# Performance work log

Hardware: AMD Instinct MI355X
Metric: run time of the kernel (lower is better)

## Reference

```python
import jax, jax.numpy as jnp
import numpy as np


def _l2norm(t, axis=-1, eps=1e-12):
    # matches torch F.normalize: x / max(||x||, eps)
    n = jnp.sqrt(jnp.sum(t * t, axis=axis, keepdims=True))
    return t / jnp.maximum(n, eps)


def setup_inputs() -> dict:
    key = jax.random.key(0)
    ks = jax.random.split(key, 5)
    B, N, C, H = 16, 4096, 768, 12
    x = jax.random.normal(ks[0], (B, N, C), dtype=jnp.float32)
    Wqkv = jax.random.normal(ks[1], (C, 3 * C), dtype=jnp.float32) * (C ** -0.5)
    bqkv = jax.random.normal(ks[2], (3 * C,), dtype=jnp.float32) * 0.02
    Wproj = jax.random.normal(ks[3], (C, C), dtype=jnp.float32) * (C ** -0.5)
    bproj = jax.random.normal(ks[4], (C,), dtype=jnp.float32) * 0.02
    temperature = jnp.ones((H, 1, 1), dtype=jnp.float32)
    return {"x": x, "Wqkv": Wqkv, "bqkv": bqkv, "Wproj": Wproj,
            "bproj": bproj, "temperature": temperature}


def reference(x, Wqkv, bqkv, Wproj, bproj, temperature):
    B, N, C = x.shape
    H = temperature.shape[0]
    Dh = C // H
    qkv = x @ Wqkv + bqkv                      # [B,N,3C]
    qkv = qkv.reshape(B, N, 3, H, Dh)
    # -> [3,B,H,Dh,N] (channels-as-tokens layout)
    qkv = jnp.transpose(qkv, (2, 0, 3, 4, 1))
    q, k, v = qkv[0], qkv[1], qkv[2]           # each [B,H,Dh,N]
    q = _l2norm(q, axis=-1)
    k = _l2norm(k, axis=-1)
    # cross-covariance over channels: [B,H,Dh,Dh]
    attn = jnp.einsum('bhdn,bhen->bhde', q, k) * temperature
    attn = jax.nn.softmax(attn, axis=-1)
    out = jnp.einsum('bhde,bhen->bhdn', attn, v)  # [B,H,Dh,N]
    out = jnp.transpose(out, (0, 3, 1, 2)).reshape(B, N, C)
    return out @ Wproj + bproj
```

## Files before the change

kernel.cpp:

```cpp
#include <hip/hip_runtime.h>

typedef __bf16 bf16x8 __attribute__((ext_vector_type(8)));
typedef float  f32x4  __attribute__((ext_vector_type(4)));
typedef unsigned short u16x8 __attribute__((ext_vector_type(8)));
typedef unsigned short u16x4 __attribute__((ext_vector_type(4)));

#define MFMA16(a, b, c) __builtin_amdgcn_mfma_f32_16x16x32_bf16((a), (b), (c), 0, 0, 0)

#define GLOAD16(g, l) __builtin_amdgcn_global_load_lds( \
    (const __attribute__((address_space(1))) void*)(g),  \
    (__attribute__((address_space(3))) void*)(l), 16, 0, 0)

__device__ __forceinline__ float bf2f(unsigned short u) {
    unsigned int x = ((unsigned int)u) << 16;
    return __builtin_bit_cast(float, x);
}
__device__ __forceinline__ unsigned short f2bf(float f) {
    unsigned int x = __builtin_bit_cast(unsigned int, f);
    x = x + 0x7FFFu + ((x >> 16) & 1u);
    return (unsigned short)(x >> 16);
}
__device__ __forceinline__ bool is_f32(const unsigned short* tf) { return tf[0] == 0; }
__device__ __forceinline__ float ldscal(const void* p, int i, bool f32m) {
    return f32m ? ((const float*)p)[i] : bf2f(((const unsigned short*)p)[i]);
}

__global__ __launch_bounds__(256)
void tr_dual(const void* __restrict__ in_, unsigned short* __restrict__ xb,
             unsigned short* __restrict__ xbT, const unsigned short* __restrict__ tf)
{
    __shared__ unsigned short T[64 * 72];
    const bool f32m = is_f32(tf);
    const int tx = blockIdx.x % 12;
    const int ty = blockIdx.x / 12;
    const int r0 = ty * 64, c0 = tx * 64;
    const int t = threadIdx.x;
#pragma unroll
    for (int s = 0; s < 2; ++s) {
        const int idx = t + s * 256;
        const int rr = idx >> 3;
        const int cc = (idx & 7) * 8;
        u16x8 v;
        if (f32m) {
            const float* inf = (const float*)in_;
            f32x4 a = *(const f32x4*)&inf[(size_t)(r0 + rr) * 768 + c0 + cc];
            f32x4 b = *(const f32x4*)&inf[(size_t)(r0 + rr) * 768 + c0 + cc + 4];
#pragma unroll
            for (int j = 0; j < 4; ++j) { v[j] = f2bf(a[j]); v[4 + j] = f2bf(b[j]); }
        } else {
            v = *(const u16x8*)&((const unsigned short*)in_)[(size_t)(r0 + rr) * 768 + c0 + cc];
        }
        *(u16x8*)&xb[(size_t)(r0 + rr) * 768 + c0 + cc] = v;
#pragma unroll
        for (int j = 0; j < 8; ++j) T[(cc + j) * 72 + rr] = v[j];
    }
    __syncthreads();
#pragma unroll
    for (int s = 0; s < 2; ++s) {
        const int idx = t + s * 256;
        const int cc = idx >> 3;
        const int rr = (idx & 7) * 8;
        u16x8 v = *(const u16x8*)&T[cc * 72 + rr];
        *(u16x8*)&xbT[(size_t)(c0 + cc) * 65536 + r0 + rr] = v;
    }
}

__global__ __launch_bounds__(256)
void tr_conv(const void* __restrict__ in_, unsigned short* __restrict__ out,
             int R, int C, int istride, const unsigned short* __restrict__ tf)
{
    __shared__ unsigned short T[64 * 72];
    const bool f32m = is_f32(tf);
    const int nct = C >> 6;
    const int tx = blockIdx.x % nct;
    const int ty = blockIdx.x / nct;
    const int r0 = ty * 64, c0 = tx * 64;
    const int t = threadIdx.x;
#pragma unroll
    for (int s = 0; s < 2; ++s) {
        const int idx = t + s * 256;
        const int rr = idx >> 3;
        const int cc = (idx & 7) * 8;
        unsigned short v[8];
        if (f32m) {
            const float* inf = (const float*)in_;
            f32x4 a = *(const f32x4*)&inf[(size_t)(r0 + rr) * istride + c0 + cc];
            f32x4 b = *(const f32x4*)&inf[(size_t)(r0 + rr) * istride + c0 + cc + 4];
#pragma unroll
            for (int j = 0; j < 4; ++j) { v[j] = f2bf(a[j]); v[4 + j] = f2bf(b[j]); }
        } else {
            u16x8 a = *(const u16x8*)&((const unsigned short*)in_)[(size_t)(r0 + rr) * istride + c0 + cc];
#pragma unroll
            for (int j = 0; j < 8; ++j) v[j] = a[j];
        }
#pragma unroll
        for (int j = 0; j < 8; ++j) T[(cc + j) * 72 + rr] = v[j];
    }
    __syncthreads();
#pragma unroll
    for (int s = 0; s < 2; ++s) {
        const int idx = t + s * 256;
        const int cc = idx >> 3;
        const int rr = (idx & 7) * 8;
        u16x8 v = *(const u16x8*)&T[cc * 72 + rr];
        *(u16x8*)&out[(size_t)(c0 + cc) * R + r0 + rr] = v;
    }
}

__global__ __launch_bounds__(256)
void conv_wv(const void* __restrict__ Wqkv, unsigned short* __restrict__ Wv_bf,
             const unsigned short* __restrict__ tf)
{
    const bool f32m = is_f32(tf);
    const int t = blockIdx.x * 256 + threadIdx.x;
    const int c = t / 96;
    const int e0 = (t % 96) * 8;
    u16x8 v;
    if (f32m) {
        const float* p = (const float*)Wqkv + (size_t)c * 2304 + 1536 + e0;
        f32x4 a = *(const f32x4*)p;
        f32x4 b = *(const f32x4*)(p + 4);
#pragma unroll
        for (int j = 0; j < 4; ++j) { v[j] = f2bf(a[j]); v[4 + j] = f2bf(b[j]); }
    } else {
        v = *(const u16x8*)&((const unsigned short*)Wqkv)[(size_t)c * 2304 + 1536 + e0];
    }
    *(u16x8*)&Wv_bf[(size_t)c * 768 + e0] = v;
}

__global__ __launch_bounds__(256)
void colsum(const unsigned short* __restrict__ xbT, float* __restrict__ s)
{
    const int b = blockIdx.x / 12;
    const int jg = blockIdx.x % 12;
    const int tid = threadIdx.x;
    const int d = tid >> 2;
    const int seg = tid & 3;
    const int j = jg * 64 + d;
    const unsigned short* p = xbT + (size_t)j * 65536 + b * 4096 + seg * 1024;
    float acc = 0.f;
    for (int i = 0; i < 128; ++i) {
        u16x8 v = *(const u16x8*)&p[i * 8];
#pragma unroll
        for (int k = 0; k < 8; ++k) acc += bf2f(v[k]);
    }
    acc += __shfl_xor(acc, 1);
    acc += __shfl_xor(acc, 2);
    if (seg == 0) s[b * 768 + j] = acc;
}

template<int MODE>
__global__ __launch_bounds__(512, 2)
void gemm256(const unsigned short* __restrict__ A,
             const unsigned short* __restrict__ BT,
             const float* __restrict__ bias,
             unsigned short* __restrict__ o0,
             float* __restrict__ oF,
             const unsigned short* __restrict__ tf)
{
    constexpr int NT = (MODE == 3) ? 64 : 12;
    constexpr size_t LDA = (MODE == 3) ? 65536 : 768;
    constexpr size_t LDB = (MODE == 3) ? 65536 : 768;
    __shared__ __align__(16) char SM[131072];

    const bool f32m = is_f32(tf);
    const int tid  = threadIdx.x;
    const int wave = tid >> 6;
    const int lane = tid & 63;
    const int wm   = wave >> 2;
    const int wn   = wave & 3;
    const int lr   = lane & 15;
    const int lq   = lane >> 4;
    const int lrh  = lr >> 1;
    const int pA   = (((lr & 1) << 2) | lq) ^ lrh;

    const int per = gridDim.x >> 3;
    const int wg  = (blockIdx.x & 7) * per + (blockIdx.x >> 3);
    int b = 0, mt, nt;
    if (MODE == 3)      { b = wg / 9;  const int r = wg % 9;  mt = r / 3; nt = r % 3; }
    else if (MODE == 4) { b = wg / 18; const int r = wg % 18; mt = r / 3; nt = r % 3; }
    else                { mt = wg / 3; nt = wg % 3; }
    const size_t m0 = (size_t)mt * 256;
    const int n0 = nt * 256;

    const unsigned short* Ab;
    const unsigned short* Bb;
    if (MODE == 3)      { Ab = A + m0 * LDA + (size_t)b * 4096;
                          Bb = A + (size_t)n0 * LDA + (size_t)b * 4096; }
    else if (MODE == 4) { Ab = A + m0 * LDA;
                          Bb = BT + (size_t)b * 589824 + (size_t)n0 * LDB; }
    else if (MODE == 1) { Ab = A + m0 * LDA;
                          Bb = BT + (m0 >> 12) * (size_t)589824 + (size_t)n0 * LDB; }
    else                { Ab = A + m0 * LDA;
                          Bb = BT + (size_t)n0 * LDB; }

    f32x4 zero = {0.f, 0.f, 0.f, 0.f};
    f32x4 acc[8][4];
#pragma unroll
    for (int i = 0; i < 8; ++i)
#pragma unroll
        for (int j = 0; j < 4; ++j) acc[i][j] = zero;

    auto STAGE_EV = [&](int mat, int kh, int t) {
        const unsigned short* g = mat ? Bb : Ab;
        const size_t ld = mat ? LDB : LDA;
        char* dst = SM + (t & 1) * 65536 + mat * 32768 + kh * 16384;
#pragma unroll
        for (int ev = 0; ev < 2; ++ev) {
            const int c = ev * 512 + tid;
            const int rp = c >> 3;
            const int chunk = (c & 7) ^ (rp & 7);
            const int srow = rp * 2 + (chunk >> 2);
            const int sk = kh * 32 + (chunk & 3) * 8;
            GLOAD16(g + (size_t)srow * ld + t * 64 + sk, dst + c * 16);
        }
    };

    STAGE_EV(0, 0, 0); STAGE_EV(1, 0, 0);
    STAGE_EV(0, 1, 0); STAGE_EV(1, 1, 0);
    STAGE_EV(0, 0, 1); STAGE_EV(1, 0, 1);

    bf16x8 af[4], bfr[4];

#define READ_B(ks) do { \
    _Pragma("unroll") for (int ni = 0; ni < 4; ++ni) \
        bfr[ni] = *(const bf16x8*)(lb + (ks) * 16384 + (wn * 32 + ni * 8 + lrh) * 128 + pA * 16); } while (0)
#define READ_A(mh, ks) do { \
    _Pragma("unroll") for (int mi = 0; mi < 4; ++mi) \
        af[mi] = *(const bf16x8*)(la + (ks) * 16384 + (wm * 64 + (mh) * 32 + mi * 8 + lrh) * 128 + pA * 16); } while (0)
#define MFMA_Q(mh) do { \
    _Pragma("unroll") for (int mi = 0; mi < 4; ++mi) \
    _Pragma("unroll") for (int ni = 0; ni < 4; ++ni) \
        acc[(mh) * 4 + mi][ni] = MFMA16(af[mi], bfr[ni], acc[(mh) * 4 + mi][ni]); } while (0)
#define PH_MID() do { \
    __builtin_amdgcn_sched_barrier(0); \
    __builtin_amdgcn_s_barrier(); \
    asm volatile("s_waitcnt lgkmcnt(0)" ::: "memory"); \
    __builtin_amdgcn_sched_barrier(0); } while (0)
#define PH_END() do { \
    __builtin_amdgcn_sched_barrier(0); \
    __builtin_amdgcn_s_barrier(); } while (0)

    for (int t = 0; t < NT; ++t) {
        const char* la = (const char*)SM + (t & 1) * 65536;
        const char* lb = la + 32768;

        if (t < NT - 1) asm volatile("s_waitcnt vmcnt(8)" ::: "memory");
        else            asm volatile("s_waitcnt vmcnt(4)" ::: "memory");
        __builtin_amdgcn_s_barrier();
        __builtin_amdgcn_sched_barrier(0);

        READ_B(0); READ_A(0, 0);
        if (t + 1 < NT) STAGE_EV(0, 1, t + 1);
        PH_MID();
        __builtin_amdgcn_s_setprio(1); MFMA_Q(0); __builtin_amdgcn_s_setprio(0);
        PH_END();

        READ_A(1, 0);
        if (t + 1 < NT) STAGE_EV(1, 1, t + 1);
        if (t < NT - 1) asm volatile("s_waitcnt vmcnt(8)" ::: "memory");
        else            asm volatile("s_waitcnt vmcnt(0)" ::: "memory");
        PH_MID();
        __builtin_amdgcn_s_setprio(1); MFMA_Q(1); __builtin_amdgcn_s_setprio(0);
        PH_END();

        READ_B(1); READ_A(0, 1);
        if (t + 2 < NT) STAGE_EV(0, 0, t + 2);
        PH_MID();
        __builtin_amdgcn_s_setprio(1); MFMA_Q(0); __builtin_amdgcn_s_setprio(0);
        PH_END();

        READ_A(1, 1);
        if (t + 2 < NT) STAGE_EV(1, 0, t + 2);
        PH_MID();
        __builtin_amdgcn_s_setprio(1); MFMA_Q(1); __builtin_amdgcn_s_setprio(0);
        PH_END();
    }
#undef READ_B
#undef READ_A
#undef MFMA_Q
#undef PH_MID
#undef PH_END

    float bb[4];
#pragma unroll
    for (int ni = 0; ni < 4; ++ni) {
        const int col = n0 + wn * 64 + ni * 16 + lr;
        bb[ni] = (MODE == 1) ? bias[(m0 >> 12) * 768 + col] : 0.f;
    }

#pragma unroll
    for (int mi = 0; mi < 8; ++mi)
#pragma unroll
        for (int ni = 0; ni < 4; ++ni)
#pragma unroll
            for (int r = 0; r < 4; ++r) {
                const size_t row = m0 + (size_t)(wm * 128 + mi * 16 + lq * 4 + r);
                const int col = n0 + wn * 64 + ni * 16 + lr;
                const float val = acc[mi][ni][r] + bb[ni];
                if (MODE == 1) {
                    if (f32m) oF[row * 768 + col] = val;
                    else      o0[row * 768 + col] = f2bf(val);
                } else if (MODE == 2) {
                    o0[row * 768 + col] = f2bf(val);
                } else if (MODE == 3) {
                    o0[(size_t)b * 589824 + row * 768 + col] = f2bf(val);
                } else {
                    o0[(size_t)b * 1179648 + row * 768 + col] = f2bf(val);
                }
            }
}

__global__ __launch_bounds__(256)
void attn2(const unsigned short* __restrict__ P,
           const unsigned short* __restrict__ WqkT,
           const float* __restrict__ s,
           const void* __restrict__ bqkv,
           const unsigned short* __restrict__ tf,
           unsigned short* __restrict__ attnT)
{
    __shared__ float S[64][64];
    __shared__ float nq[64], nk[64], uq[64], uk[64];
    __shared__ float sb[768];
    __shared__ float bkv[64];
    const bool f32m = is_f32(tf);
    const int bh = blockIdx.x;
    const int b = bh / 12, h = bh % 12;
    const unsigned short* Pq = P + (size_t)b * 1179648 + (size_t)(h * 64) * 768;
    const unsigned short* Pk = Pq + 768 * 768;
    const unsigned short* Wq = WqkT + (size_t)(h * 64) * 768;
    const unsigned short* Wk = Wq + 768 * 768;
    const int tid = threadIdx.x;
    const int wave = tid >> 6;
    const int lane = tid & 63;
    const int lr = lane & 15;
    const int lq = lane >> 4;

    for (int i = tid; i < 768; i += 256) sb[i] = s[b * 768 + i];
    if (tid < 64) bkv[tid] = ldscal(bqkv, 768 + h * 64 + tid, f32m);

    f32x4 zero = {0.f, 0.f, 0.f, 0.f};
    f32x4 acc[4][4];
#pragma unroll
    for (int i = 0; i < 4; ++i)
#pragma unroll
        for (int j = 0; j < 4; ++j) acc[i][j] = zero;

    for (int ks = 0; ks < 6; ++ks) {
        const int j0 = wave * 192 + ks * 32 + lq * 8;
        u16x8 qa[4], ka[4];
#pragma unroll
        for (int mi = 0; mi < 4; ++mi)
            qa[mi] = *(const u16x8*)&Pq[(size_t)(mi * 16 + lr) * 768 + j0];
#pragma unroll
        for (int ni = 0; ni < 4; ++ni)
            ka[ni] = *(const u16x8*)&Wk[(size_t)(ni * 16 + lr) * 768 + j0];
#pragma unroll
        for (int mi = 0; mi < 4; ++mi)
#pragma unroll
            for (int ni = 0; ni < 4; ++ni)
                acc[mi][ni] = MFMA16(__builtin_bit_cast(bf16x8, qa[mi]),
                                     __builtin_bit_cast(bf16x8, ka[ni]),
                                     acc[mi][ni]);
    }
    __syncthreads();

    for (int ww = 0; ww < 4; ++ww) {
        if (wave == ww) {
#pragma unroll
            for (int mi = 0; mi < 4; ++mi)
#pragma unroll
                for (int ni = 0; ni < 4; ++ni)
#pragma unroll
                    for (int r = 0; r < 4; ++r) {
                        const int d = mi * 16 + lq * 4 + r;
                        const int e = ni * 16 + lr;
                        if (ww == 0) S[d][e] = acc[mi][ni][r];
                        else         S[d][e] += acc[mi][ni][r];
                    }
        }
        __syncthreads();
    }

    const int d  = tid >> 2;
    const int q4 = tid & 3;
    {
        const unsigned short* pqr = Pq + (size_t)d * 768 + q4 * 192;
        const unsigned short* wqr = Wq + (size_t)d * 768 + q4 * 192;
        const unsigned short* pkr = Pk + (size_t)d * 768 + q4 * 192;
        const unsigned short* wkr = Wk + (size_t)d * 768 + q4 * 192;
        float a_nq = 0.f, a_uq = 0.f, a_nk = 0.f, a_uk = 0.f;
        for (int i = 0; i < 24; ++i) {
            u16x8 vp = *(const u16x8*)&pqr[i * 8];
            u16x8 vw = *(const u16x8*)&wqr[i * 8];
            u16x8 kp = *(const u16x8*)&pkr[i * 8];
            u16x8 kw = *(const u16x8*)&wkr[i * 8];
#pragma unroll
            for (int j = 0; j < 8; ++j) {
                const float wqv = bf2f(vw[j]);
                const float wkv = bf2f(kw[j]);
                const float sj = sb[q4 * 192 + i * 8 + j];
                a_nq += bf2f(vp[j]) * wqv;
                a_uq += sj * wqv;
                a_nk += bf2f(kp[j]) * wkv;
                a_uk += sj * wkv;
            }
        }
        a_nq += __shfl_xor(a_nq, 1); a_nq += __shfl_xor(a_nq, 2);
        a_uq += __shfl_xor(a_uq, 1); a_uq += __shfl_xor(a_uq, 2);
        a_nk += __shfl_xor(a_nk, 1); a_nk += __shfl_xor(a_nk, 2);
        a_uk += __shfl_xor(a_uk, 1); a_uk += __shfl_xor(a_uk, 2);
        if (q4 == 0) { nq[d] = a_nq; uq[d] = a_uq; nk[d] = a_nk; uk[d] = a_uk; }
    }
    __syncthreads();

    const float tv  = f32m ? ((const float*)tf)[h] : bf2f(tf[h]);
    const float bqd = ldscal(bqkv, h * 64 + d, f32m);
    const float uqd = uq[d];
    const float nqf = nq[d] + 2.f * bqd * uqd + 4096.f * bqd * bqd;
    const float qn  = fmaxf(sqrtf(fmaxf(nqf, 0.f)), 1e-12f);
    float vals[16];
    float mx = -1e30f;
#pragma unroll
    for (int i = 0; i < 16; ++i) {
        const int e = q4 * 16 + i;
        const float bke = bkv[e];
        const float nkf = nk[e] + 2.f * bke * uk[e] + 4096.f * bke * bke;
        const float kn  = fmaxf(sqrtf(fmaxf(nkf, 0.f)), 1e-12f);
        const float sv  = S[d][e] + bqd * uk[e] + uqd * bke + 4096.f * bqd * bke;
        const float val = sv / (qn * kn) * tv;
        vals[i] = val;
        mx = fmaxf(mx, val);
    }
    mx = fmaxf(mx, __shfl_xor(mx, 1));
    mx = fmaxf(mx, __shfl_xor(mx, 2));
    float sum = 0.f;
#pragma unroll
    for (int i = 0; i < 16; ++i) { vals[i] = __expf(vals[i] - mx); sum += vals[i]; }
    sum += __shfl_xor(sum, 1);
    sum += __shfl_xor(sum, 2);
    const float inv = 1.0f / sum;
#pragma unroll
    for (int i = 0; i < 16; ++i) {
        const int e = q4 * 16 + i;
        attnT[(size_t)bh * 4096 + e * 64 + d] = f2bf(vals[i] * inv);
    }
}

__global__ __launch_bounds__(512)
void mb_build(const unsigned short* __restrict__ attnT,
              const unsigned short* __restrict__ WprojT,
              unsigned short* __restrict__ MbT)
{
    const int bh = blockIdx.x;
    const int b = bh / 12, h = bh % 12;
    const int tid = threadIdx.x;
    const int wave = tid >> 6;
    const int lane = tid & 63;
    const unsigned short* At = attnT + (size_t)bh * 4096;

    f32x4 zero = {0.f, 0.f, 0.f, 0.f};
    f32x4 acc[4][6];
#pragma unroll
    for (int i = 0; i < 4; ++i)
#pragma unroll
        for (int j = 0; j < 6; ++j) acc[i][j] = zero;

    const int lr  = lane & 15;
    const int lk8 = (lane >> 4) * 8;

#pragma unroll
    for (int ks = 0; ks < 2; ++ks) {
        bf16x8 af[4], bfr[6];
#pragma unroll
        for (int mi = 0; mi < 4; ++mi)
            af[mi] = *(const bf16x8*)&At[(mi * 16 + lr) * 64 + ks * 32 + lk8];
#pragma unroll
        for (int ni = 0; ni < 6; ++ni) {
            const int j = wave * 96 + ni * 16 + lr;
            bfr[ni] = *(const bf16x8*)&WprojT[(size_t)j * 768 + h * 64 + ks * 32 + lk8];
        }
#pragma unroll
        for (int mi = 0; mi < 4; ++mi)
#pragma unroll
            for (int ni = 0; ni < 6; ++ni)
                acc[mi][ni] = MFMA16(af[mi], bfr[ni], acc[mi][ni]);
    }

#pragma unroll
    for (int mi = 0; mi < 4; ++mi)
#pragma unroll
        for (int ni = 0; ni < 6; ++ni) {
            const int e = mi * 16 + (lane >> 4) * 4;
            const int j = wave * 96 + ni * 16 + lr;
            u16x4 pk;
#pragma unroll
            for (int r = 0; r < 4; ++r) pk[r] = f2bf(acc[mi][ni][r]);
            *(u16x4*)&MbT[(size_t)b * 589824 + (size_t)j * 768 + h * 64 + e] = pk;
        }
}

__global__ __launch_bounds__(256)
void beff_k(const unsigned short* __restrict__ MbT,
            const void* __restrict__ bqkv, const void* __restrict__ bp,
            float* __restrict__ beff, const unsigned short* __restrict__ tf)
{
    __shared__ float bv[768];
    const bool f32m = is_f32(tf);
    for (int i = threadIdx.x; i < 768; i += 256) bv[i] = ldscal(bqkv, 1536 + i, f32m);
    __syncthreads();
    const int t = blockIdx.x * 256 + threadIdx.x;
    const int b = t / 768, j = t % 768;
    float s = ldscal(bp, j, f32m);
    const unsigned short* row = MbT + (size_t)b * 589824 + (size_t)j * 768;
    for (int e8 = 0; e8 < 96; ++e8) {
        u16x8 m = *(const u16x8*)&row[e8 * 8];
#pragma unroll
        for (int jj = 0; jj < 8; ++jj) s += bf2f(m[jj]) * bv[e8 * 8 + jj];
    }
    beff[t] = s;
}

extern "C" void kernel_launch(void* const* d_in, const int* in_sizes, int n_in,
                              void* d_out, int out_size, void* d_ws, size_t ws_size,
                              hipStream_t stream)
{
    const void* x    = d_in[0];
    const void* Wqkv = d_in[1];
    const void* bqkv = d_in[2];
    const void* Wp   = d_in[3];
    const void* bp   = d_in[4];
    const unsigned short* tf = (const unsigned short*)d_in[5];

    char* w = (char*)d_ws;
    unsigned short* xbT    = (unsigned short*)(w);
    unsigned short* xb     = (unsigned short*)(w + 100663296);
    unsigned short* G      = (unsigned short*)(w + 201326592);
    unsigned short* P      = (unsigned short*)(w + 220200960);
    unsigned short* PT     = (unsigned short*)(w + 257949696);
    unsigned short* MbT    = (unsigned short*)(w + 276824064);
    unsigned short* WqkT   = (unsigned short*)(w + 295698432);
    unsigned short* Wv_bf  = (unsigned short*)(w + 298057728);
    unsigned short* WprojT = (unsigned short*)(w + 299237376);
    unsigned short* attnT  = (unsigned short*)(w + 300417024);
    float*          sB     = (float*)(w + 301989888);
    float*          beff   = (float*)(w + 302039040);

    tr_dual<<<dim3(12288), dim3(256), 0, stream>>>(x, xb, xbT, tf);
    tr_conv<<<dim3(288),  dim3(256), 0, stream>>>(Wqkv, WqkT, 768, 1536, 2304, tf);
    conv_wv<<<dim3(288),  dim3(256), 0, stream>>>(Wqkv, Wv_bf, tf);
    tr_conv<<<dim3(144),  dim3(256), 0, stream>>>(Wp, WprojT, 768, 768, 768, tf);
    colsum <<<dim3(192),  dim3(256), 0, stream>>>(xbT, sB);

    gemm256<3><<<dim3(144), dim3(512), 0, stream>>>(xbT, nullptr, nullptr, G, nullptr, tf);
    gemm256<4><<<dim3(288), dim3(512), 0, stream>>>(WqkT, G, nullptr, P, nullptr, tf);
    attn2<<<dim3(192), dim3(256), 0, stream>>>(P, WqkT, sB, bqkv, tf, attnT);
    mb_build<<<dim3(192), dim3(512), 0, stream>>>(attnT, WprojT, MbT);
    gemm256<2><<<dim3(144), dim3(512), 0, stream>>>(MbT, Wv_bf, nullptr, PT, nullptr, tf);
    beff_k<<<dim3(48), dim3(256), 0, stream>>>(MbT, bqkv, bp, beff, tf);
    gemm256<1><<<dim3(768), dim3(512), 0, stream>>>(xb, PT, beff,
        (unsigned short*)d_out, (float*)d_out, tf);
}
```

Baseline: 453.8 us.

## Fuse colsum into transpose, merge weight prep kernels, add simpler two-phase K=768 GEMM

Computes the per-batch column sums inside the x transpose kernel from the LDS tile, using atomicAdd into a zeroed buffer. This removes the separate colsum pass that re-read xbT. The three weight conversion and transpose kernels are merged into one launch. The K=768 GEMMs now use a new simpler double-buffered two-phase kernel, while the long-K Gram GEMM keeps the eight-phase pipeline. The trade-offs are atomics, a memset, and possibly less latency hiding in the new GEMM loop.

```diff
diff --git a/kernel.cpp b/kernel.cpp
--- a/kernel.cpp
+++ b/kernel.cpp
@@ -27,7 +27,8 @@
 
 __global__ __launch_bounds__(256)
 void tr_dual(const void* __restrict__ in_, unsigned short* __restrict__ xb,
-             unsigned short* __restrict__ xbT, const unsigned short* __restrict__ tf)
+             unsigned short* __restrict__ xbT, float* __restrict__ sB,
+             const unsigned short* __restrict__ tf)
 {
     __shared__ unsigned short T[64 * 72];
     const bool f32m = is_f32(tf);
@@ -63,17 +64,25 @@
         u16x8 v = *(const u16x8*)&T[cc * 72 + rr];
         *(u16x8*)&xbT[(size_t)(c0 + cc) * 65536 + r0 + rr] = v;
     }
-}
-
-__global__ __launch_bounds__(256)
-void tr_conv(const void* __restrict__ in_, unsigned short* __restrict__ out,
-             int R, int C, int istride, const unsigned short* __restrict__ tf)
-{
-    __shared__ unsigned short T[64 * 72];
-    const bool f32m = is_f32(tf);
+    {
+        const int col = t >> 2;
+        const int seg = t & 3;
+        float s = 0.f;
+#pragma unroll
+        for (int r = 0; r < 16; ++r) s += bf2f(T[col * 72 + seg * 16 + r]);
+        s += __shfl_xor(s, 1);
+        s += __shfl_xor(s, 2);
+        if (seg == 0) atomicAdd(&sB[(r0 >> 12) * 768 + c0 + col], s);
+    }
+}
+
+__device__ __forceinline__ void tr_tile(const void* in_, unsigned short* out,
+                                        int R, int C, int istride,
+                                        int bid, bool f32m, unsigned short* T)
+{
     const int nct = C >> 6;
-    const int tx = blockIdx.x % nct;
-    const int ty = blockIdx.x / nct;
+    const int tx = bid % nct;
+    const int ty = bid / nct;
     const int r0 = ty * 64, c0 = tx * 64;
     const int t = threadIdx.x;
 #pragma unroll
@@ -108,62 +117,183 @@
 }
 
 __global__ __launch_bounds__(256)
-void conv_wv(const void* __restrict__ Wqkv, unsigned short* __restrict__ Wv_bf,
-             const unsigned short* __restrict__ tf)
-{
+void wprep(const void* __restrict__ Wqkv, const void* __restrict__ Wp,
+           unsigned short* __restrict__ WqkT, unsigned short* __restrict__ Wv_bf,
+           unsigned short* __restrict__ WprojT, const unsigned short* __restrict__ tf)
+{
+    __shared__ unsigned short T[64 * 72];
     const bool f32m = is_f32(tf);
-    const int t = blockIdx.x * 256 + threadIdx.x;
-    const int c = t / 96;
-    const int e0 = (t % 96) * 8;
-    u16x8 v;
-    if (f32m) {
-        const float* p = (const float*)Wqkv + (size_t)c * 2304 + 1536 + e0;
-        f32x4 a = *(const f32x4*)p;
-        f32x4 b = *(const f32x4*)(p + 4);
-#pragma unroll
-        for (int j = 0; j < 4; ++j) { v[j] = f2bf(a[j]); v[4 + j] = f2bf(b[j]); }
+    const int bid = blockIdx.x;
+    if (bid < 288) {
+        tr_tile(Wqkv, WqkT, 768, 1536, 2304, bid, f32m, T);
+    } else if (bid < 576) {
+        const int t = (bid - 288) * 256 + threadIdx.x;
+        const int c = t / 96;
+        const int e0 = (t % 96) * 8;
+        u16x8 v;
+        if (f32m) {
+            const float* p = (const float*)Wqkv + (size_t)c * 2304 + 1536 + e0;
+            f32x4 a = *(const f32x4*)p;
+            f32x4 b = *(const f32x4*)(p + 4);
+#pragma unroll
+            for (int j = 0; j < 4; ++j) { v[j] = f2bf(a[j]); v[4 + j] = f2bf(b[j]); }
+        } else {
+            v = *(const u16x8*)&((const unsigned short*)Wqkv)[(size_t)c * 2304 + 1536 + e0];
+        }
+        *(u16x8*)&Wv_bf[(size_t)c * 768 + e0] = v;
     } else {
-        v = *(const u16x8*)&((const unsigned short*)Wqkv)[(size_t)c * 2304 + 1536 + e0];
-    }
-    *(u16x8*)&Wv_bf[(size_t)c * 768 + e0] = v;
-}
-
-__global__ __launch_bounds__(256)
-void colsum(const unsigned short* __restrict__ xbT, float* __restrict__ s)
-{
-    const int b = blockIdx.x / 12;
-    const int jg = blockIdx.x % 12;
-    const int tid = threadIdx.x;
-    const int d = tid >> 2;
-    const int seg = tid & 3;
-    const int j = jg * 64 + d;
-    const unsigned short* p = xbT + (size_t)j * 65536 + b * 4096 + seg * 1024;
-    float acc = 0.f;
-    for (int i = 0; i < 128; ++i) {
-        u16x8 v = *(const u16x8*)&p[i * 8];
-#pragma unroll
-        for (int k = 0; k < 8; ++k) acc += bf2f(v[k]);
-    }
-    acc += __shfl_xor(acc, 1);
-    acc += __shfl_xor(acc, 2);
-    if (seg == 0) s[b * 768 + j] = acc;
+        tr_tile(Wp, WprojT, 768, 768, 768, bid - 576, f32m, T);
+    }
 }
 
 template<int MODE>
 __global__ __launch_bounds__(512, 2)
-void gemm256(const unsigned short* __restrict__ A,
+void gemm2ph(const unsigned short* __restrict__ A,
              const unsigned short* __restrict__ BT,
              const float* __restrict__ bias,
              unsigned short* __restrict__ o0,
              float* __restrict__ oF,
              const unsigned short* __restrict__ tf)
 {
-    constexpr int NT = (MODE == 3) ? 64 : 12;
-    constexpr size_t LDA = (MODE == 3) ? 65536 : 768;
-    constexpr size_t LDB = (MODE == 3) ? 65536 : 768;
+    constexpr int K = 768, NT = 12;
     __shared__ __align__(16) char SM[131072];
+    unsigned short* lds = (unsigned short*)SM;
 
     const bool f32m = is_f32(tf);
+    const int tid  = threadIdx.x;
+    const int wave = tid >> 6;
+    const int lane = tid & 63;
+    const int wm   = wave >> 2;
+    const int wn   = wave & 3;
+    const int lr   = lane & 15;
+    const int lq   = lane >> 4;
+
+    const int per = gridDim.x >> 3;
+    const int wg  = (blockIdx.x & 7) * per + (blockIdx.x >> 3);
+    int b = 0, mt, nt;
+    if (MODE == 4) { b = wg / 18; const int r = wg % 18; mt = r / 3; nt = r % 3; }
+    else           { mt = wg / 3; nt = wg % 3; }
+    const size_t m0 = (size_t)mt * 256;
+    const int n0 = nt * 256;
+
+    const unsigned short* Ab = A + m0 * K;
+    const unsigned short* Bb;
+    if (MODE == 1)      Bb = BT + (m0 >> 12) * (size_t)589824 + (size_t)n0 * K;
+    else if (MODE == 4) Bb = BT + (size_t)b * 589824 + (size_t)n0 * K;
+    else                Bb = BT + (size_t)n0 * K;
+
+    f32x4 zero = {0.f, 0.f, 0.f, 0.f};
+    f32x4 acc[8][4];
+#pragma unroll
+    for (int i = 0; i < 8; ++i)
+#pragma unroll
+        for (int j = 0; j < 4; ++j) acc[i][j] = zero;
+
+    auto STAGE = [&](int t) {
+        unsigned short* la_ = lds + (t & 1) * 32768;
+        unsigned short* lb_ = la_ + 16384;
+        const unsigned short* ga = Ab + t * 64;
+        const unsigned short* gb = Bb + t * 64;
+#pragma unroll
+        for (int it = 0; it < 4; ++it) {
+            const int c = it * 512 + tid;
+            const int row = c >> 3;
+            const int gs = (c & 7) ^ (row & 7);
+            GLOAD16(ga + (size_t)row * K + gs * 8, la_ + c * 8);
+        }
+#pragma unroll
+        for (int it = 0; it < 4; ++it) {
+            const int c = it * 512 + tid;
+            const int row = c >> 3;
+            const int gs = (c & 7) ^ (row & 7);
+            GLOAD16(gb + (size_t)row * K + gs * 8, lb_ + c * 8);
+        }
+    };
+
+    STAGE(0);
+    STAGE(1);
+
+    for (int t = 0; t < NT; ++t) {
+        if (t + 1 < NT) asm volatile("s_waitcnt vmcnt(8)" ::: "memory");
+        else            asm volatile("s_waitcnt vmcnt(0)" ::: "memory");
+        __builtin_amdgcn_s_barrier();
+        __builtin_amdgcn_sched_barrier(0);
+
+        const char* la = (const char*)(lds + (t & 1) * 32768);
+        const char* lb = la + 32768;
+
+        bf16x8 bfr[4][2];
+#pragma unroll
+        for (int ni = 0; ni < 4; ++ni)
+#pragma unroll
+            for (int ks = 0; ks < 2; ++ks) {
+                const int row = wn * 64 + ni * 16 + lr;
+                const int s   = ks * 4 + lq;
+                bfr[ni][ks] = *(const bf16x8*)(lb + row * 128 + ((s ^ (row & 7)) << 4));
+            }
+#pragma unroll
+        for (int mh = 0; mh < 2; ++mh) {
+            bf16x8 af[4][2];
+#pragma unroll
+            for (int mi = 0; mi < 4; ++mi)
+#pragma unroll
+                for (int ks = 0; ks < 2; ++ks) {
+                    const int row = wm * 128 + mh * 64 + mi * 16 + lr;
+                    const int s   = ks * 4 + lq;
+                    af[mi][ks] = *(const bf16x8*)(la + row * 128 + ((s ^ (row & 7)) << 4));
+                }
+            __builtin_amdgcn_s_setprio(1);
+#pragma unroll
+            for (int mi = 0; mi < 4; ++mi)
+#pragma unroll
+                for (int ni = 0; ni < 4; ++ni)
+#pragma unroll
+                    for (int ks = 0; ks < 2; ++ks)
+                        acc[mh * 4 + mi][ni] = MFMA16(af[mi][ks], bfr[ni][ks], acc[mh * 4 + mi][ni]);
+            __builtin_amdgcn_s_setprio(0);
+        }
+
+        __builtin_amdgcn_sched_barrier(0);
+        __builtin_amdgcn_s_barrier();
+        if (t + 2 < NT) STAGE(t + 2);
+    }
+
+    float bb[4];
+#pragma unroll
+    for (int ni = 0; ni < 4; ++ni) {
+        const int col = n0 + wn * 64 + ni * 16 + lr;
+        bb[ni] = (MODE == 1) ? bias[(m0 >> 12) * 768 + col] : 0.f;
+    }
+
+#pragma unroll
+    for (int mi = 0; mi < 8; ++mi)
+#pragma unroll
+        for (int ni = 0; ni < 4; ++ni)
+#pragma unroll
+            for (int r = 0; r < 4; ++r) {
+                const size_t row = m0 + (size_t)(wm * 128 + mi * 16 + lq * 4 + r);
+                const int col = n0 + wn * 64 + ni * 16 + lr;
+                const float val = acc[mi][ni][r] + bb[ni];
+                if (MODE == 1) {
+                    if (f32m) oF[row * 768 + col] = val;
+                    else      o0[row * 768 + col] = f2bf(val);
+                } else if (MODE == 2) {
+                    o0[row * 768 + col] = f2bf(val);
+                } else {
+                    o0[(size_t)b * 1179648 + row * 768 + col] = f2bf(val);
+                }
+            }
+}
+
+__global__ __launch_bounds__(512, 2)
+void gemm8ph(const unsigned short* __restrict__ A,
+             unsigned short* __restrict__ G,
+             const unsigned short* __restrict__ tf)
+{
+    constexpr int NT = 64;
+    constexpr size_t LD = 65536;
+    __shared__ __align__(16) char SM[131072];
+
     const int tid  = threadIdx.x;
     const int wave = tid >> 6;
     const int lane = tid & 63;
@@ -176,23 +306,14 @@
 
     const int per = gridDim.x >> 3;
     const int wg  = (blockIdx.x & 7) * per + (blockIdx.x >> 3);
-    int b = 0, mt, nt;
-    if (MODE == 3)      { b = wg / 9;  const int r = wg % 9;  mt = r / 3; nt = r % 3; }
-    else if (MODE == 4) { b = wg / 18; const int r = wg % 18; mt = r / 3; nt = r % 3; }
-    else                { mt = wg / 3; nt = wg % 3; }
+    const int b = wg / 9;
+    const int r9 = wg % 9;
+    const int mt = r9 / 3, nt = r9 % 3;
     const size_t m0 = (size_t)mt * 256;
     const int n0 = nt * 256;
 
-    const unsigned short* Ab;
-    const unsigned short* Bb;
-    if (MODE == 3)      { Ab = A + m0 * LDA + (size_t)b * 4096;
-                          Bb = A + (size_t)n0 * LDA + (size_t)b * 4096; }
-    else if (MODE == 4) { Ab = A + m0 * LDA;
-                          Bb = BT + (size_t)b * 589824 + (size_t)n0 * LDB; }
-    else if (MODE == 1) { Ab = A + m0 * LDA;
-                          Bb = BT + (m0 >> 12) * (size_t)589824 + (size_t)n0 * LDB; }
-    else                { Ab = A + m0 * LDA;
-                          Bb = BT + (size_t)n0 * LDB; }
+    const unsigned short* Ab = A + m0 * LD + (size_t)b * 4096;
+    const unsigned short* Bb = A + (size_t)n0 * LD + (size_t)b * 4096;
 
     f32x4 zero = {0.f, 0.f, 0.f, 0.f};
     f32x4 acc[8][4];
@@ -203,7 +324,6 @@
 
     auto STAGE_EV = [&](int mat, int kh, int t) {
         const unsigned short* g = mat ? Bb : Ab;
-        const size_t ld = mat ? LDB : LDA;
         char* dst = SM + (t & 1) * 65536 + mat * 32768 + kh * 16384;
 #pragma unroll
         for (int ev = 0; ev < 2; ++ev) {
@@ -212,7 +332,7 @@
             const int chunk = (c & 7) ^ (rp & 7);
             const int srow = rp * 2 + (chunk >> 2);
             const int sk = kh * 32 + (chunk & 3) * 8;
-            GLOAD16(g + (size_t)srow * ld + t * 64 + sk, dst + c * 16);
+            GLOAD16(g + (size_t)srow * LD + t * 64 + sk, dst + c * 16);
         }
     };
 
@@ -282,13 +402,6 @@
 #undef PH_MID
 #undef PH_END
 
-    float bb[4];
-#pragma unroll
-    for (int ni = 0; ni < 4; ++ni) {
-        const int col = n0 + wn * 64 + ni * 16 + lr;
-        bb[ni] = (MODE == 1) ? bias[(m0 >> 12) * 768 + col] : 0.f;
-    }
-
 #pragma unroll
     for (int mi = 0; mi < 8; ++mi)
 #pragma unroll
@@ -297,17 +410,7 @@
             for (int r = 0; r < 4; ++r) {
                 const size_t row = m0 + (size_t)(wm * 128 + mi * 16 + lq * 4 + r);
                 const int col = n0 + wn * 64 + ni * 16 + lr;
-                const float val = acc[mi][ni][r] + bb[ni];
-                if (MODE == 1) {
-                    if (f32m) oF[row * 768 + col] = val;
-                    else      o0[row * 768 + col] = f2bf(val);
-                } else if (MODE == 2) {
-                    o0[row * 768 + col] = f2bf(val);
-                } else if (MODE == 3) {
-                    o0[(size_t)b * 589824 + row * 768 + col] = f2bf(val);
-                } else {
-                    o0[(size_t)b * 1179648 + row * 768 + col] = f2bf(val);
-                }
+                G[(size_t)b * 589824 + row * 768 + col] = f2bf(acc[mi][ni][r]);
             }
 }
 
@@ -546,18 +649,16 @@
     float*          sB     = (float*)(w + 301989888);
     float*          beff   = (float*)(w + 302039040);
 
-    tr_dual<<<dim3(12288), dim3(256), 0, stream>>>(x, xb, xbT, tf);
-    tr_conv<<<dim3(288),  dim3(256), 0, stream>>>(Wqkv, WqkT, 768, 1536, 2304, tf);
-    conv_wv<<<dim3(288),  dim3(256), 0, stream>>>(Wqkv, Wv_bf, tf);
-    tr_conv<<<dim3(144),  dim3(256), 0, stream>>>(Wp, WprojT, 768, 768, 768, tf);
-    colsum <<<dim3(192),  dim3(256), 0, stream>>>(xbT, sB);
-
-    gemm256<3><<<dim3(144), dim3(512), 0, stream>>>(xbT, nullptr, nullptr, G, nullptr, tf);
-    gemm256<4><<<dim3(288), dim3(512), 0, stream>>>(WqkT, G, nullptr, P, nullptr, tf);
+    hipMemsetAsync(sB, 0, 16 * 768 * sizeof(float), stream);
+    tr_dual<<<dim3(12288), dim3(256), 0, stream>>>(x, xb, xbT, sB, tf);
+    wprep<<<dim3(720), dim3(256), 0, stream>>>(Wqkv, Wp, WqkT, Wv_bf, WprojT, tf);
+
+    gemm8ph<<<dim3(144), dim3(512), 0, stream>>>(xbT, G, tf);
+    gemm2ph<4><<<dim3(288), dim3(512), 0, stream>>>(WqkT, G, nullptr, P, nullptr, tf);
     attn2<<<dim3(192), dim3(256), 0, stream>>>(P, WqkT, sB, bqkv, tf, attnT);
     mb_build<<<dim3(192), dim3(512), 0, stream>>>(attnT, WprojT, MbT);
-    gemm256<2><<<dim3(144), dim3(512), 0, stream>>>(MbT, Wv_bf, nullptr, PT, nullptr, tf);
+    gemm2ph<2><<<dim3(144), dim3(512), 0, stream>>>(MbT, Wv_bf, nullptr, PT, nullptr, tf);
     beff_k<<<dim3(48), dim3(256), 0, stream>>>(MbT, bqkv, bp, beff, tf);
-    gemm256<1><<<dim3(768), dim3(512), 0, stream>>>(xb, PT, beff,
+    gemm2ph<1><<<dim3(768), dim3(512), 0, stream>>>(xb, PT, beff,
         (unsigned short*)d_out, (float*)d_out, tf);
 }
```

Result: no change. 450.2 us (-0.8%).
